# Kernel optimization log

Measured on AMD Instinct MI355X. Metric: run time of the kernel, lower is better.

The kernel has to match this reference:

```python
import jax, jax.numpy as jnp
import numpy as np

B, S, DIM = 4, 3968, 512
H, HD = 8, 64
CHUNK, NPM, MEM = 496, 32, 1024  # MEM == NPM + 2*CHUNK (required by module's EMA update broadcast)


def _lin(k, din, dout):
    kw, kb = jax.random.split(k)
    w = jax.random.normal(kw, (din, dout), jnp.float32) / np.sqrt(din)
    b = jax.random.normal(kb, (dout,), jnp.float32) * 0.01
    return w, b


def setup_inputs() -> dict:
    key = jax.random.key(0)
    ks = jax.random.split(key, 12)
    inp = {}
    inp["x"] = jax.random.normal(ks[0], (B, S, DIM), jnp.float32)
    inp["persistent_memory"] = jax.random.normal(ks[1], (NPM, DIM), jnp.float32)
    # outer query projection
    inp["Wq_out"], inp["bq_out"] = _lin(ks[2], DIM, DIM)
    # NeuralMemory projections
    inp["mk_w"], inp["mk_b"] = _lin(ks[3], DIM, DIM)
    inp["mv_w"], inp["mv_b"] = _lin(ks[4], DIM, DIM)
    inp["mq_w"], inp["mq_b"] = _lin(ks[5], DIM, DIM)
    # TitanAttention (standard MHA: q/k/v to H*HD, out proj back to DIM)
    inp["aq_w"], inp["aq_b"] = _lin(ks[6], DIM, H * HD)
    inp["ak_w"], inp["ak_b"] = _lin(ks[7], DIM, H * HD)
    inp["av_w"], inp["av_b"] = _lin(ks[8], DIM, H * HD)
    inp["ao_w"], inp["ao_b"] = _lin(ks[9], H * HD, DIM)
    return inp


def reference(x, persistent_memory, Wq_out, bq_out,
              mk_w, mk_b, mv_w, mv_b, mq_w, mq_b,
              aq_w, aq_b, ak_w, ak_b, av_w, av_b, ao_w, ao_b):
    Bn, Sn, D = x.shape
    nch = Sn // CHUNK
    inv_sqrt_d = 1.0 / np.sqrt(D).astype(np.float32)
    inv_sqrt_hd = 1.0 / np.sqrt(HD).astype(np.float32)

    def retrieve(mem, q):
        # mem: [B, MEM, D], q: [B, L, D]
        qp = q @ mq_w + mq_b
        k = mem @ mk_w + mk_b
        v = mem @ mv_w + mv_b
        sc = jnp.einsum('bqd,bmd->bqm', qp, k) * inv_sqrt_d
        a = jax.nn.softmax(sc, axis=-1)
        return jnp.einsum('bqm,bmd->bqd', a, v)

    def mha(t):
        # t: [B, L, D] -> [B, L, D]; dropout inactive (eval)
        Bm, L, _ = t.shape
        q = (t @ aq_w + aq_b).reshape(Bm, L, H, HD)
        k = (t @ ak_w + ak_b).reshape(Bm, L, H, HD)
        v = (t @ av_w + av_b).reshape(Bm, L, H, HD)
        sc = jnp.einsum('bqhd,bkhd->bhqk', q, k) * inv_sqrt_hd
        a = jax.nn.softmax(sc, axis=-1)
        o = jnp.einsum('bhqk,bkhd->bqhd', a, v).reshape(Bm, L, H * HD)
        return o @ ao_w + ao_b

    pm = jnp.broadcast_to(persistent_memory[None], (Bn, NPM, D))
    chunks = x.reshape(Bn, nch, CHUNK, D).transpose(1, 0, 2, 3)  # [nch, B, C, D]
    mem0 = jnp.zeros((Bn, MEM, D), x.dtype)

    def step(mem, chunk):
        query = chunk @ Wq_out + bq_out
        hist = retrieve(mem, query)                              # [B, C, D]
        combined = jnp.concatenate([pm, hist, chunk], axis=1)    # [B, MEM, D]
        attended = mha(combined)
        mem2 = 0.9 * mem + 0.1 * attended                        # EMA update
        mout = retrieve(mem2, attended)
        out = (attended * mout)[:, -CHUNK:]                      # keep last chunk slice
        return mem2, out

    _, outs = jax.lax.scan(step, mem0, chunks)                   # outs: [nch, B, C, D]
    return outs.transpose(1, 0, 2, 3).reshape(Bn, Sn, D)
```

## Files before the change

### kernel.cpp

```cpp
#include <hip/hip_runtime.h>
#include <hip/hip_fp16.h>


typedef __attribute__((ext_vector_type(8))) short short8;
typedef __attribute__((ext_vector_type(4))) float f32x4;

static __device__ __forceinline__ unsigned short f32_bf16(float f) {
  unsigned int u = __float_as_uint(f);
  u += 0x7FFFu + ((u >> 16) & 1u);
  return (unsigned short)(u >> 16);
}
static __device__ __forceinline__ unsigned pk(float lo, float hi) {
  return (unsigned)f32_bf16(lo) | ((unsigned)f32_bf16(hi) << 16);
}

template<int BM, int BN, int ATY, int BTY, int CTY, bool GUARD, bool BIAS>
__global__ __launch_bounds__(256) void gemm2(
    const void* __restrict__ Ap, long long Asb, long long Ash, int Ars,
    const void* __restrict__ Bp, long long Bsb, long long Bsh, int Brs,
    void* __restrict__ Cp, long long Csb, long long Csh, int Crs,
    void* __restrict__ Cp2, int csplit, void* __restrict__ Cp3,
    const float* __restrict__ bias, float scale, int M, int Kdim, int Hh)
{
  constexpr int LDP = 72;
  constexpr int WN = (BN >= 128) ? 2 : (BM >= 128 ? 1 : 2);
  constexpr int WM = 4 / WN;
  constexpr int MI = BM / (WM * 16);
  constexpr int NI = BN / (WN * 16);
  constexpr int AP = BM / 32;
  constexpr int BP = BN / 32;

  __shared__ unsigned short As[2][BM][LDP];
  __shared__ unsigned short Bs[2][BN][LDP];

  const int tid  = threadIdx.x;
  const int lane = tid & 63;
  const int w    = tid >> 6;
  const int wm   = w / WN, wn = w % WN;
  const int z    = blockIdx.z;
  const int zb   = z / Hh, zh = z - zb * Hh;
  const int m0   = blockIdx.x * BM;
  const int n0   = blockIdx.y * BN;
  const int lrow = lane & 15;
  const int lkB  = (lane >> 4) * 8;
  const int srow = tid >> 3;
  const int scol = (tid & 7) * 8;

  const float*          Af  = (const float*)Ap          + zb * Asb + zh * Ash;
  const unsigned short* Ahp = (const unsigned short*)Ap + zb * Asb + zh * Ash;
  const float*          Bf  = (const float*)Bp          + zb * Bsb + zh * Bsh;
  const unsigned short* Bhp = (const unsigned short*)Bp + zb * Bsb + zh * Bsh;

  float4 afl[AP][2]; uint4 ahl[AP];
  float4 bfl[BP][2]; uint4 bhl[BP];

  auto loadT = [&](int k0) {
    #pragma unroll
    for (int p = 0; p < AP; ++p) {
      const int row = srow + p * 32;
      const bool ok = !GUARD || (m0 + row) < M;
      if constexpr (ATY == 0) {
        if (ok) {
          const float* s = Af + (long long)(m0 + row) * Ars + k0 + scol;
          afl[p][0] = *(const float4*)s;
          afl[p][1] = *(const float4*)(s + 4);
        } else {
          afl[p][0] = make_float4(0.f,0.f,0.f,0.f);
          afl[p][1] = make_float4(0.f,0.f,0.f,0.f);
        }
      } else {
        ahl[p] = ok ? *(const uint4*)(Ahp + (long long)(m0 + row) * Ars + k0 + scol)
                    : make_uint4(0u,0u,0u,0u);
      }
    }
    #pragma unroll
    for (int p = 0; p < BP; ++p) {
      const int row = srow + p * 32;
      if constexpr (BTY == 0) {
        const float* s = Bf + (long long)(n0 + row) * Brs + k0 + scol;
        bfl[p][0] = *(const float4*)s;
        bfl[p][1] = *(const float4*)(s + 4);
      } else {
        bhl[p] = *(const uint4*)(Bhp + (long long)(n0 + row) * Brs + k0 + scol);
      }
    }
  };
  auto writeT = [&](int buf) {
    #pragma unroll
    for (int p = 0; p < AP; ++p) {
      const int row = srow + p * 32;
      uint4 u;
      if constexpr (ATY == 0) {
        u.x = pk(afl[p][0].x, afl[p][0].y); u.y = pk(afl[p][0].z, afl[p][0].w);
        u.z = pk(afl[p][1].x, afl[p][1].y); u.w = pk(afl[p][1].z, afl[p][1].w);
      } else u = ahl[p];
      *(uint4*)(&As[buf][row][scol]) = u;
    }
    #pragma unroll
    for (int p = 0; p < BP; ++p) {
      const int row = srow + p * 32;
      uint4 u;
      if constexpr (BTY == 0) {
        u.x = pk(bfl[p][0].x, bfl[p][0].y); u.y = pk(bfl[p][0].z, bfl[p][0].w);
        u.z = pk(bfl[p][1].x, bfl[p][1].y); u.w = pk(bfl[p][1].z, bfl[p][1].w);
      } else u = bhl[p];
      *(uint4*)(&Bs[buf][row][scol]) = u;
    }
  };

  f32x4 acc[MI][NI] = {};

  loadT(0);
  writeT(0);
  __syncthreads();

  const int NT = Kdim >> 6;
  int cur = 0;
  for (int t = 0; t < NT; ++t) {
    const bool more = (t + 1) < NT;
    if (more) loadT((t + 1) << 6);

    short8 a8[MI][2], b8[NI][2];
    #pragma unroll
    for (int mi = 0; mi < MI; ++mi) {
      const unsigned short* r = &As[cur][wm * (MI * 16) + mi * 16 + lrow][lkB];
      a8[mi][0] = *(const short8*)r;
      a8[mi][1] = *(const short8*)(r + 32);
    }
    #pragma unroll
    for (int ni = 0; ni < NI; ++ni) {
      const unsigned short* r = &Bs[cur][wn * (NI * 16) + ni * 16 + lrow][lkB];
      b8[ni][0] = *(const short8*)r;
      b8[ni][1] = *(const short8*)(r + 32);
    }
    #pragma unroll
    for (int kk = 0; kk < 2; ++kk)
      #pragma unroll
      for (int mi = 0; mi < MI; ++mi)
        #pragma unroll
        for (int ni = 0; ni < NI; ++ni)
          acc[mi][ni] = __builtin_amdgcn_mfma_f32_16x16x32_bf16(a8[mi][kk], b8[ni][kk], acc[mi][ni], 0, 0, 0);

    if (more) writeT(cur ^ 1);
    __syncthreads();
    cur ^= 1;
  }

  float*          Cf  = (float*)Cp          + zb * Csb + zh * Csh;
  unsigned short* Chn = (unsigned short*)Cp + zb * Csb + zh * Csh;
  unsigned short* Ch2 = (unsigned short*)Cp2;
  unsigned short* Kb3 = (unsigned short*)Cp3;
  const bool trside = (CTY == 4 || CTY == 5) ? (n0 >= csplit) : false;

  #pragma unroll
  for (int ni = 0; ni < NI; ++ni) {
    const int col = n0 + wn * (NI * 16) + ni * 16 + lrow;
    const float bv = BIAS ? bias[col] : 0.0f;
    #pragma unroll
    for (int mi = 0; mi < MI; ++mi) {
      const int rbase = m0 + wm * (MI * 16) + mi * 16 + ((lane >> 4) << 2);
      if constexpr (CTY == 5) {
        ushort4 vt;
        #pragma unroll
        for (int r = 0; r < 4; ++r) {
          const int row = rbase + r;
          const float proj = acc[mi][ni][r] * scale + bv;
          const long long midx = (long long)row * Crs + col;
          const float v = 0.9f * Cf[midx] + 0.1f * proj;
          Cf[midx] = v;
          if (!trside) Kb3[(long long)row * 512 + col] = f32_bf16(v);
          else ((unsigned short*)&vt)[r] = f32_bf16(v);
        }
        if (trside)
          *(ushort4*)(&Ch2[(long long)(rbase >> 10) * 524288
                           + (long long)(col - csplit) * 1024 + (rbase & 1023)]) = vt;
      } else if constexpr (CTY == 6) {
        const float* ATTp = (const float*)Cp2;
        float* Of = (float*)Cp;
        #pragma unroll
        for (int r = 0; r < 4; ++r) {
          const int row = rbase + r;
          if (row < M) {
            const float v = acc[mi][ni][r] * scale;
            const float a = ATTp[((long long)zb * 1024 + 528 + row) * 512 + col];
            Of[((long long)zb * 3968 + (long long)csplit * 496 + row) * 512 + col] = v * a;
          }
        }
      } else if (trside) {
        ushort4 v;
        v.x = f32_bf16(acc[mi][ni][0] * scale + bv);
        v.y = f32_bf16(acc[mi][ni][1] * scale + bv);
        v.z = f32_bf16(acc[mi][ni][2] * scale + bv);
        v.w = f32_bf16(acc[mi][ni][3] * scale + bv);
        *(ushort4*)(&Ch2[(long long)(rbase >> 10) * 524288
                         + (long long)(col - csplit) * 1024 + (rbase & 1023)]) = v;
      } else {
        #pragma unroll
        for (int r = 0; r < 4; ++r) {
          const int row = rbase + r;
          if (!GUARD || row < M) {
            const float v = acc[mi][ni][r] * scale + bv;
            if constexpr (CTY == 0)      Cf [(long long)row * Crs + col] = v;
            else                         Chn[(long long)row * Crs + col] = f32_bf16(v);
          }
        }
      }
    }
  }
}

__global__ __launch_bounds__(256) void flash_mha(
    const unsigned short* __restrict__ QK, const unsigned short* __restrict__ Vt,
    unsigned short* __restrict__ OH)
{
  __shared__ unsigned short Ks[128][72];
  __shared__ unsigned short Vs[64][136];
  __shared__ unsigned short Ps[64][136];

  const int tid = threadIdx.x, lane = tid & 63, w = tid >> 6;
  const int f = blockIdx.x;
  const int xcd = f & 7, j = f >> 3;
  const int bh = xcd + 8 * (j >> 4);
  const int qt = j & 15;
  const int b = bh >> 3, h = bh & 7;
  const int q0 = qt * 64;
  const unsigned short* Qp = QK + (long long)b * 1048576 + h * 64;
  const unsigned short* Kp = Qp + 512;
  const unsigned short* Vp = Vt + (long long)b * 524288 + (long long)(h * 64) * 1024;
  unsigned short* Op = OH + (long long)b * 524288 + h * 64;

  const int lr = lane & 15, g = lane >> 4, lk = g * 8;
  const int wq = w * 16;

  short8 qb[2];
  qb[0] = *(const short8*)(Qp + (long long)(q0 + wq + lr) * 1024 + lk);
  qb[1] = *(const short8*)(Qp + (long long)(q0 + wq + lr) * 1024 + 32 + lk);

  const int krow = tid >> 1, kcol = (tid & 1) * 32;
  const int vrow = tid >> 2, vcol = (tid & 3) * 32;

  uint4 kl[4], vl[4];
  auto loadKV = [&](int kt) {
    #pragma unroll
    for (int jj = 0; jj < 4; ++jj)
      kl[jj] = *(const uint4*)(Kp + (long long)(kt * 128 + krow) * 1024 + kcol + jj * 8);
    #pragma unroll
    for (int jj = 0; jj < 4; ++jj)
      vl[jj] = *(const uint4*)(Vp + (long long)vrow * 1024 + kt * 128 + vcol + jj * 8);
  };
  auto writeKV = [&]() {
    #pragma unroll
    for (int jj = 0; jj < 4; ++jj) *(uint4*)(&Ks[krow][kcol + jj * 8]) = kl[jj];
    #pragma unroll
    for (int jj = 0; jj < 4; ++jj) *(uint4*)(&Vs[vrow][vcol + jj * 8]) = vl[jj];
  };

  loadKV(0); writeKV();
  __syncthreads();

  f32x4 acc[4] = {};
  float m = -1e30f, l = 0.f;

  for (int kt = 0; kt < 8; ++kt) {
    const bool more = kt < 7;
    if (more) loadKV(kt + 1);

    f32x4 s[8] = {};
    #pragma unroll
    for (int ks = 0; ks < 2; ++ks)
      #pragma unroll
      for (int ni = 0; ni < 8; ++ni) {
        const short8 ka = *(const short8*)(&Ks[ni * 16 + lr][ks * 32 + lk]);
        s[ni] = __builtin_amdgcn_mfma_f32_16x16x32_bf16(ka, qb[ks], s[ni], 0, 0, 0);
      }

    float rm = -1e30f;
    #pragma unroll
    for (int ni = 0; ni < 8; ++ni)
      #pragma unroll
      for (int r = 0; r < 4; ++r) { s[ni][r] *= 0.125f; rm = fmaxf(rm, s[ni][r]); }
    rm = fmaxf(rm, __shfl_xor(rm, 16));
    rm = fmaxf(rm, __shfl_xor(rm, 32));

    const float mn = fmaxf(m, rm);
    const float al = __expf(m - mn);
    m = mn;
    float ls = 0.f;
    #pragma unroll
    for (int ni = 0; ni < 8; ++ni)
      #pragma unroll
      for (int r = 0; r < 4; ++r) { s[ni][r] = __expf(s[ni][r] - m); ls += s[ni][r]; }
    ls += __shfl_xor(ls, 16);
    ls += __shfl_xor(ls, 32);
    l = l * al + ls;
    #pragma unroll
    for (int nd = 0; nd < 4; ++nd)
      #pragma unroll
      for (int r = 0; r < 4; ++r) acc[nd][r] *= al;

    #pragma unroll
    for (int ni = 0; ni < 8; ++ni)
      #pragma unroll
      for (int r = 0; r < 4; ++r)
        Ps[wq + lr][ni * 16 + (g << 2) + r] = f32_bf16(s[ni][r]);

    #pragma unroll
    for (int ks2 = 0; ks2 < 4; ++ks2) {
      const short8 pb = *(const short8*)(&Ps[wq + lr][ks2 * 32 + lk]);
      #pragma unroll
      for (int nd = 0; nd < 4; ++nd) {
        const short8 va = *(const short8*)(&Vs[nd * 16 + lr][ks2 * 32 + lk]);
        acc[nd] = __builtin_amdgcn_mfma_f32_16x16x32_bf16(va, pb, acc[nd], 0, 0, 0);
      }
    }

    __syncthreads();
    if (more) { writeKV(); __syncthreads(); }
  }

  unsigned short (*Os)[72] = (unsigned short (*)[72])&Ks[0][0];
  const float inv = 1.0f / l;
  #pragma unroll
  for (int nd = 0; nd < 4; ++nd)
    #pragma unroll
    for (int r = 0; r < 4; ++r)
      Os[wq + lr][nd * 16 + (g << 2) + r] = f32_bf16(acc[nd][r] * inv);
  __syncthreads();
  const int orow = tid >> 2, ocol = (tid & 3) * 16;
  const uint4 u0 = *(const uint4*)(&Os[orow][ocol]);
  const uint4 u1 = *(const uint4*)(&Os[orow][ocol + 8]);
  *(uint4*)(Op + (long long)(q0 + orow) * 512 + ocol) = u0;
  *(uint4*)(Op + (long long)(q0 + orow) * 512 + ocol + 8) = u1;
}

struct TP7 { const float* s[7]; unsigned short* d[7]; };
__global__ __launch_bounds__(256) void transpose7(TP7 tp)
{
  __shared__ float tile[32][33];
  const float* in = tp.s[blockIdx.z];
  unsigned short* out = tp.d[blockIdx.z];
  const int c0 = blockIdx.x * 32, r0 = blockIdx.y * 32;
  const int xx = threadIdx.x & 31, ys = threadIdx.x >> 5;
  #pragma unroll
  for (int yy = ys; yy < 32; yy += 8)
    tile[yy][xx] = in[(long long)(r0 + yy) * 512 + c0 + xx];
  __syncthreads();
  #pragma unroll
  for (int yy = ys; yy < 32; yy += 8)
    out[(long long)(c0 + yy) * 512 + r0 + xx] = f32_bf16(tile[xx][yy]);
}

__global__ __launch_bounds__(256) void softmax_rows_bf(
    const float* __restrict__ buf, unsigned short* __restrict__ obuf,
    int rowsPerZ, long long zStride)
{
  const int gr   = blockIdx.x * 4 + (threadIdx.x >> 6);
  const int lane = threadIdx.x & 63;
  const int z = gr / rowsPerZ;
  const int i = gr - z * rowsPerZ;
  const float* pf = buf + (long long)z * zStride + (long long)i * 1024 + lane * 16;
  float v[16];
  #pragma unroll
  for (int j = 0; j < 4; ++j) {
    const float4 f = ((const float4*)pf)[j];
    v[4*j+0] = f.x; v[4*j+1] = f.y; v[4*j+2] = f.z; v[4*j+3] = f.w;
  }
  float mx = v[0];
  #pragma unroll
  for (int j = 1; j < 16; ++j) mx = fmaxf(mx, v[j]);
  #pragma unroll
  for (int d = 32; d; d >>= 1) mx = fmaxf(mx, __shfl_xor(mx, d));
  float s = 0.0f;
  #pragma unroll
  for (int j = 0; j < 16; ++j) { v[j] = __expf(v[j] - mx); s += v[j]; }
  #pragma unroll
  for (int d = 32; d; d >>= 1) s += __shfl_xor(s, d);
  const float inv = 1.0f / s;
  unsigned short* ph = obuf + (long long)z * zStride + (long long)i * 1024 + lane * 16;
  unsigned uu[8];
  #pragma unroll
  for (int j = 0; j < 8; ++j) uu[j] = pk(v[2*j] * inv, v[2*j+1] * inv);
  ((uint4*)ph)[0] = make_uint4(uu[0], uu[1], uu[2], uu[3]);
  ((uint4*)ph)[1] = make_uint4(uu[4], uu[5], uu[6], uu[7]);
}

__global__ __launch_bounds__(256) void copy_pm_bf(const float* __restrict__ pm, unsigned short* __restrict__ comb)
{
  const int idx = blockIdx.x * 256 + threadIdx.x;
  const int b = idx >> 11, e = idx & 2047;
  const int row = e >> 6, d8 = (e & 63) * 8;
  const float* s = pm + row * 512 + d8;
  const float4 f0 = *(const float4*)s;
  const float4 f1 = *(const float4*)(s + 4);
  uint4 u; u.x = pk(f0.x, f0.y); u.y = pk(f0.z, f0.w); u.z = pk(f1.x, f1.y); u.w = pk(f1.z, f1.w);
  *(uint4*)(comb + (long long)b * 524288 + row * 512 + d8) = u;
}

__global__ __launch_bounds__(256) void copy_chunk_bf(const float* __restrict__ x, unsigned short* __restrict__ comb, int ci)
{
  const int idx = blockIdx.x * 256 + threadIdx.x;
  const int b = idx / 31744, e = idx % 31744;
  const int row = e >> 6, d8 = (e & 63) * 8;
  const float* s = x + ((long long)b * 3968 + ci * 496 + row) * 512 + d8;
  const float4 f0 = *(const float4*)s;
  const float4 f1 = *(const float4*)(s + 4);
  uint4 u; u.x = pk(f0.x, f0.y); u.y = pk(f0.z, f0.w); u.z = pk(f1.x, f1.y); u.w = pk(f1.z, f1.w);
  *(uint4*)(comb + (long long)b * 524288 + (528 + row) * 512 + d8) = u;
}

__global__ __launch_bounds__(256) void init_kv(const float* __restrict__ mkb, const float* __restrict__ mvb,
                                               float* __restrict__ master, unsigned short* __restrict__ Kb)
{
  const int idx = blockIdx.x * 256 + threadIdx.x;
  const int c4 = (idx & 255) * 4;
  const long long row = idx >> 8;
  const float4 v = *(const float4*)((c4 < 512) ? (mkb + c4) : (mvb + c4 - 512));
  *(float4*)(master + row * 1024 + c4) = v;
  if (c4 < 512) {
    ushort4 h; h.x = f32_bf16(v.x); h.y = f32_bf16(v.y); h.z = f32_bf16(v.z); h.w = f32_bf16(v.w);
    *(ushort4*)(Kb + row * 512 + c4) = h;
  }
}

__global__ __launch_bounds__(256) void init_vt(const float* __restrict__ mvb, unsigned short* __restrict__ VT)
{
  const int idx = blockIdx.x * 256 + threadIdx.x;
  const int k8 = (idx & 127) * 8;
  const int d  = (idx >> 7) & 511;
  const int b  = idx >> 16;
  const unsigned short hv = f32_bf16(mvb[d]);
  const ushort4 h4 = make_ushort4(hv, hv, hv, hv);
  unsigned short* dst = VT + (long long)b * 524288 + (long long)d * 1024 + k8;
  *(ushort4*)dst = h4; *(ushort4*)(dst + 4) = h4;
}

__global__ __launch_bounds__(256) void fuse_bias(const float* __restrict__ bq, const float* __restrict__ mq,
                                                 const float* __restrict__ mqb, float* __restrict__ bqm)
{
  const int c = blockIdx.x * 256 + threadIdx.x;
  float s = mqb[c];
  for (int j = 0; j < 512; ++j) s += bq[j] * mq[j * 512 + c];
  bqm[c] = s;
}

extern "C" void kernel_launch(void* const* d_in, const int* in_sizes, int n_in,
                              void* d_out, int out_size, void* d_ws, size_t ws_size,
                              hipStream_t stream)
{
  (void)in_sizes; (void)n_in; (void)out_size; (void)ws_size;
  const float* x   = (const float*)d_in[0];
  const float* pm  = (const float*)d_in[1];
  const float* Wq  = (const float*)d_in[2];
  const float* bq  = (const float*)d_in[3];
  const float* mkw = (const float*)d_in[4];
  const float* mkb = (const float*)d_in[5];
  const float* mvw = (const float*)d_in[6];
  const float* mvb = (const float*)d_in[7];
  const float* mqw = (const float*)d_in[8];
  const float* mqb = (const float*)d_in[9];
  const float* aqw = (const float*)d_in[10];
  const float* aqb = (const float*)d_in[11];
  const float* akw = (const float*)d_in[12];
  const float* akb = (const float*)d_in[13];
  const float* avw = (const float*)d_in[14];
  const float* avb = (const float*)d_in[15];
  const float* aow = (const float*)d_in[16];
  const float* aob = (const float*)d_in[17];
  float* out = (float*)d_out;

  char* wsp = (char*)d_ws;
  size_t off = 0;
  auto alloc = [&](size_t b) -> void* { void* p = wsp + off; off += (b + 255) & ~(size_t)255; return p; };

  unsigned short* WTmq = (unsigned short*)alloc(524288);
  unsigned short* WKV  = (unsigned short*)alloc(1048576);
  unsigned short* WQKV = (unsigned short*)alloc(1572864);
  unsigned short* WTao = (unsigned short*)alloc(524288);
  unsigned short* Wqm  = (unsigned short*)alloc(524288);
  float* bkv  = (float*)alloc(4096);
  float* bqkv = (float*)alloc(6144);
  float* bqm  = (float*)alloc(2048);
  float*          master = (float*)alloc(16777216);
  unsigned short* Kb   = (unsigned short*)alloc(4194304);
  unsigned short* VT   = (unsigned short*)alloc(4194304);
  unsigned short* VTm  = (unsigned short*)alloc(4194304);
  unsigned short* QP1  = (unsigned short*)alloc(16252928);
  unsigned short* QP   = (unsigned short*)alloc(2031616);
  unsigned short* comb = (unsigned short*)alloc(4194304);
  unsigned short* QKb  = (unsigned short*)alloc(8388608);
  unsigned short* OH   = (unsigned short*)alloc(4194304);
  float*          ATT  = (float*)alloc(8388608);
  float*          SC   = (float*)alloc(8126464);
  unsigned short* SCb  = (unsigned short*)alloc(4063232);

  const long long XBS = 2031616, BS = 524288, QBS = 253952;
  const long long SCB = 507904;
  const float sr = 0.044194173824159216f;

  TP7 tp;
  tp.s[0] = mqw; tp.d[0] = WTmq;
  tp.s[1] = mkw; tp.d[1] = WKV;
  tp.s[2] = mvw; tp.d[2] = WKV + 262144;
  tp.s[3] = aqw; tp.d[3] = WQKV;
  tp.s[4] = akw; tp.d[4] = WQKV + 262144;
  tp.s[5] = avw; tp.d[5] = WQKV + 524288;
  tp.s[6] = aow; tp.d[6] = WTao;
  transpose7<<<dim3(16,16,7),256,0,stream>>>(tp);
  gemm2<64,64,1,0,2,false,false><<<dim3(8,8,1),256,0,stream>>>(
    WTmq, 0, 0, 512, Wq, 0, 0, 512, Wqm, 0, 0, 512,
    nullptr, 0, nullptr, nullptr, 1.0f, 512, 512, 1);
  fuse_bias<<<2,256,0,stream>>>(bq, mqw, mqb, bqm);
  gemm2<128,64,0,1,2,false,true><<<dim3(124,8,1),256,0,stream>>>(
    x, 0, 0, 512, Wqm, 0, 0, 512,
    QP1, 0, 0, 512, nullptr, 0, nullptr, bqm, 1.0f, 15872, 512, 1);
  hipMemcpyAsync(bkv,        mkb, 2048, hipMemcpyDeviceToDevice, stream);
  hipMemcpyAsync(bkv  + 512, mvb, 2048, hipMemcpyDeviceToDevice, stream);
  hipMemcpyAsync(bqkv,       aqb, 2048, hipMemcpyDeviceToDevice, stream);
  hipMemcpyAsync(bqkv + 512, akb, 2048, hipMemcpyDeviceToDevice, stream);
  hipMemcpyAsync(bqkv +1024, avb, 2048, hipMemcpyDeviceToDevice, stream);
  init_kv<<<4096,256,0,stream>>>(mkb, mvb, master, Kb);
  init_vt<<<1024,256,0,stream>>>(mvb, VT);
  copy_pm_bf<<<32,256,0,stream>>>(pm, comb);

  for (int ci = 0; ci < 8; ++ci) {
    copy_chunk_bf<<<496,256,0,stream>>>(x, comb, ci);

    gemm2<64,64,1,1,0,true,false><<<dim3(8,16,4),256,0,stream>>>(
      QP1 + (long long)ci * 253952, XBS, 0, 512, Kb, BS, 0, 512,
      SC, SCB, 0, 1024, nullptr, 0, nullptr, nullptr, sr, 496, 512, 1);
    softmax_rows_bf<<<496,256,0,stream>>>(SC, SCb, 496, SCB);
    gemm2<64,64,1,1,2,true,false><<<dim3(8,8,4),256,0,stream>>>(
      SCb, SCB, 0, 1024, VT, BS, 0, 1024,
      comb + 32 * 512, BS, 0, 512, nullptr, 0, nullptr, nullptr, 1.0f, 496, 1024, 1);

    gemm2<128,64,1,1,4,false,true><<<dim3(32,24,1),256,0,stream>>>(
      comb, 0, 0, 512, WQKV, 0, 0, 512,
      QKb, 0, 0, 1024, VTm, 1024, nullptr, bqkv, 1.0f, 4096, 512, 1);
    flash_mha<<<512,256,0,stream>>>(QKb, VTm, OH);
    gemm2<128,64,1,1,0,false,true><<<dim3(32,8,1),256,0,stream>>>(
      OH, 0, 0, 512, WTao, 0, 0, 512,
      ATT, 0, 0, 512, nullptr, 0, nullptr, aob, 1.0f, 4096, 512, 1);

    gemm2<128,64,0,1,5,false,true><<<dim3(32,16,1),256,0,stream>>>(
      ATT, 0, 0, 512, WKV, 0, 0, 512,
      master, 0, 0, 1024, VT, 512, Kb, bkv, 1.0f, 4096, 512, 1);

    gemm2<64,64,0,1,2,true,true><<<dim3(8,8,4),256,0,stream>>>(
      ATT + 528 * 512, BS, 0, 512, WTmq, 0, 0, 512,
      QP, QBS, 0, 512, nullptr, 0, nullptr, mqb, 1.0f, 496, 512, 1);
    gemm2<64,64,1,1,0,true,false><<<dim3(8,16,4),256,0,stream>>>(
      QP, QBS, 0, 512, Kb, BS, 0, 512,
      SC, SCB, 0, 1024, nullptr, 0, nullptr, nullptr, sr, 496, 512, 1);
    softmax_rows_bf<<<496,256,0,stream>>>(SC, SCb, 496, SCB);
    gemm2<64,64,1,1,6,true,false><<<dim3(8,8,4),256,0,stream>>>(
      SCb, SCB, 0, 1024, VT, BS, 0, 1024,
      out, 0, 0, 512, ATT, ci, nullptr, nullptr, 1.0f, 496, 1024, 1);
  }
}
```

Measured before the change: 1.369 ms.

## Fold attention output projection into memory K/V and query weights

Precomputes combined weights ao_w·mk_w/mv_w and ao_w·mq_w with fused biases, so the per-chunk memory K/V update and the query projection read the MHA head output directly instead of the materialised attended tensor. The full output projection now runs only on the last 496 rows of each batch that the final product needs. Chunk and persistent-memory bf16 staging is hoisted out of the loop into one batched copy across all 8 chunks, at the cost of a larger workspace buffer. The refactored weights are rounded to bf16 once, which changes rounding relative to the two-step projection.

Measured after the change: 1.346 ms. About the same (-1.7%).

```diff
diff --git a/kernel.cpp b/kernel.cpp
--- a/kernel.cpp
+++ b/kernel.cpp
@@ -182,7 +182,7 @@
           const int row = rbase + r;
           if (row < M) {
             const float v = acc[mi][ni][r] * scale;
-            const float a = ATTp[((long long)zb * 1024 + 528 + row) * 512 + col];
+            const float a = ATTp[((long long)zb * 496 + row) * 512 + col];
             Of[((long long)zb * 3968 + (long long)csplit * 496 + row) * 512 + col] = v * a;
           }
         }
@@ -384,8 +384,9 @@
   ((uint4*)ph)[1] = make_uint4(uu[4], uu[5], uu[6], uu[7]);
 }
 
-__global__ __launch_bounds__(256) void copy_pm_bf(const float* __restrict__ pm, unsigned short* __restrict__ comb)
-{
+__global__ __launch_bounds__(256) void copy_pm8(const float* __restrict__ pm, unsigned short* __restrict__ comb8)
+{
+  const int ci = blockIdx.y;
   const int idx = blockIdx.x * 256 + threadIdx.x;
   const int b = idx >> 11, e = idx & 2047;
   const int row = e >> 6, d8 = (e & 63) * 8;
@@ -393,11 +394,12 @@
   const float4 f0 = *(const float4*)s;
   const float4 f1 = *(const float4*)(s + 4);
   uint4 u; u.x = pk(f0.x, f0.y); u.y = pk(f0.z, f0.w); u.z = pk(f1.x, f1.y); u.w = pk(f1.z, f1.w);
-  *(uint4*)(comb + (long long)b * 524288 + row * 512 + d8) = u;
-}
-
-__global__ __launch_bounds__(256) void copy_chunk_bf(const float* __restrict__ x, unsigned short* __restrict__ comb, int ci)
-{
+  *(uint4*)(comb8 + (long long)ci * 2097152 + (long long)b * 524288 + row * 512 + d8) = u;
+}
+
+__global__ __launch_bounds__(256) void copy_chunk8(const float* __restrict__ x, unsigned short* __restrict__ comb8)
+{
+  const int ci = blockIdx.y;
   const int idx = blockIdx.x * 256 + threadIdx.x;
   const int b = idx / 31744, e = idx % 31744;
   const int row = e >> 6, d8 = (e & 63) * 8;
@@ -405,7 +407,7 @@
   const float4 f0 = *(const float4*)s;
   const float4 f1 = *(const float4*)(s + 4);
   uint4 u; u.x = pk(f0.x, f0.y); u.y = pk(f0.z, f0.w); u.z = pk(f1.x, f1.y); u.w = pk(f1.z, f1.w);
-  *(uint4*)(comb + (long long)b * 524288 + (528 + row) * 512 + d8) = u;
+  *(uint4*)(comb8 + (long long)ci * 2097152 + (long long)b * 524288 + (528 + row) * 512 + d8) = u;
 }
 
 __global__ __launch_bounds__(256) void init_kv(const float* __restrict__ mkb, const float* __restrict__ mvb,
@@ -441,6 +443,20 @@
   float s = mqb[c];
   for (int j = 0; j < 512; ++j) s += bq[j] * mq[j * 512 + c];
   bqm[c] = s;
+}
+
+__global__ __launch_bounds__(256) void fuse_bias2(const float* __restrict__ aob,
+                                                  const float* __restrict__ mkw, const float* __restrict__ mkb,
+                                                  const float* __restrict__ mvw, const float* __restrict__ mvb,
+                                                  float* __restrict__ baokv)
+{
+  const int c = blockIdx.x * 256 + threadIdx.x;
+  const float* w  = (c < 512) ? mkw : mvw;
+  const float* bb = (c < 512) ? mkb : mvb;
+  const int cc = c & 511;
+  float s = bb[cc];
+  for (int j = 0; j < 512; ++j) s += aob[j] * w[j * 512 + cc];
+  baokv[c] = s;
 }
 
 extern "C" void kernel_launch(void* const* d_in, const int* in_sizes, int n_in,
@@ -472,24 +488,27 @@
   size_t off = 0;
   auto alloc = [&](size_t b) -> void* { void* p = wsp + off; off += (b + 255) & ~(size_t)255; return p; };
 
-  unsigned short* WTmq = (unsigned short*)alloc(524288);
-  unsigned short* WKV  = (unsigned short*)alloc(1048576);
-  unsigned short* WQKV = (unsigned short*)alloc(1572864);
-  unsigned short* WTao = (unsigned short*)alloc(524288);
-  unsigned short* Wqm  = (unsigned short*)alloc(524288);
-  float* bkv  = (float*)alloc(4096);
-  float* bqkv = (float*)alloc(6144);
-  float* bqm  = (float*)alloc(2048);
+  unsigned short* WTmq  = (unsigned short*)alloc(524288);
+  unsigned short* WKV   = (unsigned short*)alloc(1048576);
+  unsigned short* WQKV  = (unsigned short*)alloc(1572864);
+  unsigned short* WTao  = (unsigned short*)alloc(524288);
+  unsigned short* Wqm   = (unsigned short*)alloc(524288);
+  unsigned short* WaoKV = (unsigned short*)alloc(1048576);
+  unsigned short* Waomq = (unsigned short*)alloc(524288);
+  float* bqkv  = (float*)alloc(6144);
+  float* bqm   = (float*)alloc(2048);
+  float* baokv = (float*)alloc(4096);
+  float* baomq = (float*)alloc(2048);
   float*          master = (float*)alloc(16777216);
   unsigned short* Kb   = (unsigned short*)alloc(4194304);
   unsigned short* VT   = (unsigned short*)alloc(4194304);
   unsigned short* VTm  = (unsigned short*)alloc(4194304);
   unsigned short* QP1  = (unsigned short*)alloc(16252928);
   unsigned short* QP   = (unsigned short*)alloc(2031616);
-  unsigned short* comb = (unsigned short*)alloc(4194304);
+  unsigned short* comb8= (unsigned short*)alloc(33554432);
   unsigned short* QKb  = (unsigned short*)alloc(8388608);
   unsigned short* OH   = (unsigned short*)alloc(4194304);
-  float*          ATT  = (float*)alloc(8388608);
+  float*          ATT  = (float*)alloc(4063232);
   float*          SC   = (float*)alloc(8126464);
   unsigned short* SCb  = (unsigned short*)alloc(4063232);
 
@@ -509,21 +528,28 @@
   gemm2<64,64,1,0,2,false,false><<<dim3(8,8,1),256,0,stream>>>(
     WTmq, 0, 0, 512, Wq, 0, 0, 512, Wqm, 0, 0, 512,
     nullptr, 0, nullptr, nullptr, 1.0f, 512, 512, 1);
+  gemm2<64,64,1,0,2,false,false><<<dim3(16,8,1),256,0,stream>>>(
+    WKV, 0, 0, 512, aow, 0, 0, 512, WaoKV, 0, 0, 512,
+    nullptr, 0, nullptr, nullptr, 1.0f, 1024, 512, 1);
+  gemm2<64,64,1,0,2,false,false><<<dim3(8,8,1),256,0,stream>>>(
+    WTmq, 0, 0, 512, aow, 0, 0, 512, Waomq, 0, 0, 512,
+    nullptr, 0, nullptr, nullptr, 1.0f, 512, 512, 1);
   fuse_bias<<<2,256,0,stream>>>(bq, mqw, mqb, bqm);
+  fuse_bias<<<2,256,0,stream>>>(aob, mqw, mqb, baomq);
+  fuse_bias2<<<4,256,0,stream>>>(aob, mkw, mkb, mvw, mvb, baokv);
   gemm2<128,64,0,1,2,false,true><<<dim3(124,8,1),256,0,stream>>>(
     x, 0, 0, 512, Wqm, 0, 0, 512,
     QP1, 0, 0, 512, nullptr, 0, nullptr, bqm, 1.0f, 15872, 512, 1);
-  hipMemcpyAsync(bkv,        mkb, 2048, hipMemcpyDeviceToDevice, stream);
-  hipMemcpyAsync(bkv  + 512, mvb, 2048, hipMemcpyDeviceToDevice, stream);
   hipMemcpyAsync(bqkv,       aqb, 2048, hipMemcpyDeviceToDevice, stream);
   hipMemcpyAsync(bqkv + 512, akb, 2048, hipMemcpyDeviceToDevice, stream);
   hipMemcpyAsync(bqkv +1024, avb, 2048, hipMemcpyDeviceToDevice, stream);
   init_kv<<<4096,256,0,stream>>>(mkb, mvb, master, Kb);
   init_vt<<<1024,256,0,stream>>>(mvb, VT);
-  copy_pm_bf<<<32,256,0,stream>>>(pm, comb);
+  copy_pm8<<<dim3(32,8),256,0,stream>>>(pm, comb8);
+  copy_chunk8<<<dim3(496,8),256,0,stream>>>(x, comb8);
 
   for (int ci = 0; ci < 8; ++ci) {
-    copy_chunk_bf<<<496,256,0,stream>>>(x, comb, ci);
+    unsigned short* comb = comb8 + (long long)ci * 2097152;
 
     gemm2<64,64,1,1,0,true,false><<<dim3(8,16,4),256,0,stream>>>(
       QP1 + (long long)ci * 253952, XBS, 0, 512, Kb, BS, 0, 512,
@@ -537,17 +563,17 @@
       comb, 0, 0, 512, WQKV, 0, 0, 512,
       QKb, 0, 0, 1024, VTm, 1024, nullptr, bqkv, 1.0f, 4096, 512, 1);
     flash_mha<<<512,256,0,stream>>>(QKb, VTm, OH);
-    gemm2<128,64,1,1,0,false,true><<<dim3(32,8,1),256,0,stream>>>(
-      OH, 0, 0, 512, WTao, 0, 0, 512,
-      ATT, 0, 0, 512, nullptr, 0, nullptr, aob, 1.0f, 4096, 512, 1);
-
-    gemm2<128,64,0,1,5,false,true><<<dim3(32,16,1),256,0,stream>>>(
-      ATT, 0, 0, 512, WKV, 0, 0, 512,
-      master, 0, 0, 1024, VT, 512, Kb, bkv, 1.0f, 4096, 512, 1);
-
-    gemm2<64,64,0,1,2,true,true><<<dim3(8,8,4),256,0,stream>>>(
-      ATT + 528 * 512, BS, 0, 512, WTmq, 0, 0, 512,
-      QP, QBS, 0, 512, nullptr, 0, nullptr, mqb, 1.0f, 496, 512, 1);
+
+    gemm2<128,64,1,1,5,false,true><<<dim3(32,16,1),256,0,stream>>>(
+      OH, 0, 0, 512, WaoKV, 0, 0, 512,
+      master, 0, 0, 1024, VT, 512, Kb, baokv, 1.0f, 4096, 512, 1);
+    gemm2<64,64,1,1,2,true,true><<<dim3(8,8,4),256,0,stream>>>(
+      OH + 528 * 512, BS, 0, 512, Waomq, 0, 0, 512,
+      QP, QBS, 0, 512, nullptr, 0, nullptr, baomq, 1.0f, 496, 512, 1);
+    gemm2<64,64,1,1,0,true,true><<<dim3(8,8,4),256,0,stream>>>(
+      OH + 528 * 512, BS, 0, 512, WTao, 0, 0, 512,
+      ATT, QBS, 0, 512, nullptr, 0, nullptr, aob, 1.0f, 496, 512, 1);
+
     gemm2<64,64,1,1,0,true,false><<<dim3(8,16,4),256,0,stream>>>(
       QP, QBS, 0, 512, Kb, BS, 0, 512,
       SC, SCB, 0, 1024, nullptr, 0, nullptr, nullptr, sr, 496, 512, 1);
```
